# Optimization experiments

Measured on AMD Instinct MI355X. Metric: run time of the kernel, lower is better.

The kernel has to match this reference:

```python
import jax, jax.numpy as jnp
import numpy as np

N_OBJ, N_EVT, N_EDGE, N_MAIN = 50000, 100000, 500000, 25000
OBJ_DIM, EVT_DIM = 256, 256


def setup_inputs() -> dict:
    key = jax.random.key(0)
    ks = jax.random.split(key, 12)
    s = 1.0 / np.sqrt(OBJ_DIM)
    return {
        "object_X": jax.random.normal(ks[0], (N_OBJ, OBJ_DIM), jnp.float32),
        "event_X": jax.random.normal(ks[1], (N_EVT, EVT_DIM), jnp.float32),
        "lc_obj_idx": jax.random.randint(ks[2], (N_EDGE,), 0, N_OBJ),
        "lc_evt_idx": jax.random.randint(ks[3], (N_EDGE,), 0, N_EVT),
        "main_idx": jax.random.randint(ks[4], (N_MAIN,), 0, N_OBJ),
        # lifecycle_proj: Linear(event_dim, obj_dim)
        "W_proj": jax.random.uniform(ks[5], (OBJ_DIM, EVT_DIM), jnp.float32, -s, s),
        "b_proj": jax.random.uniform(ks[6], (OBJ_DIM,), jnp.float32, -s, s),
        # GRUCell(obj_dim, obj_dim): weight_ih/hh are [3*H, H]
        "W_ih": jax.random.uniform(ks[7], (3 * OBJ_DIM, OBJ_DIM), jnp.float32, -s, s),
        "b_ih": jax.random.uniform(ks[8], (3 * OBJ_DIM,), jnp.float32, -s, s),
        "W_hh": jax.random.uniform(ks[9], (3 * OBJ_DIM, OBJ_DIM), jnp.float32, -s, s),
        "b_hh": jax.random.uniform(ks[10], (3 * OBJ_DIM,), jnp.float32, -s, s),
    }


def reference(object_X, event_X, lc_obj_idx, lc_evt_idx, main_idx,
              W_proj, b_proj, W_ih, b_ih, W_hh, b_hh):
    n_obj = object_X.shape[0]
    # gather event feats, linear + ReLU  -> [E, obj_dim]
    proj = jax.nn.relu(event_X[lc_evt_idx] @ W_proj.T + b_proj)
    # scatter_mean over target objects (empty slots -> 0, like torch_scatter)
    sums = jax.ops.segment_sum(proj, lc_obj_idx, num_segments=n_obj)
    cnt = jax.ops.segment_sum(jnp.ones((lc_obj_idx.shape[0],), proj.dtype),
                              lc_obj_idx, num_segments=n_obj)
    profile = sums / jnp.maximum(cnt, 1.0)[:, None]  # [N_obj, obj_dim]
    # GRUCell(profile, object_X)
    gi = profile @ W_ih.T + b_ih   # [N_obj, 3H]
    gh = object_X @ W_hh.T + b_hh  # [N_obj, 3H]
    i_r, i_z, i_n = jnp.split(gi, 3, axis=-1)
    h_r, h_z, h_n = jnp.split(gh, 3, axis=-1)
    r = jax.nn.sigmoid(i_r + h_r)
    z = jax.nn.sigmoid(i_z + h_z)
    n = jnp.tanh(i_n + r * h_n)
    updated = (1.0 - z) * n + z * object_X
    # masked blend: only main objects take updated values
    mask = jnp.zeros((n_obj, 1), object_X.dtype).at[main_idx].set(1.0)
    return mask * updated + (1.0 - mask) * object_X
```

## Files before the change

kernel.cpp:

```cpp
#include <hip/hip_runtime.h>

typedef unsigned short u16;
typedef __attribute__((ext_vector_type(8))) short bf16x8;
typedef __attribute__((ext_vector_type(4))) float f32x4;

struct __align__(8) u16x4_t { u16 x, y, z, w; };

__device__ __forceinline__ float b2f(u16 b) {
  union { unsigned u; float f; } v; v.u = ((unsigned)b) << 16; return v.f;
}
__device__ __forceinline__ u16 f2b(float f) {
  union { float f; unsigned u; } v; v.f = f;
  unsigned r = v.u + 0x7fffu + ((v.u >> 16) & 1u);
  return (u16)(r >> 16);
}

__global__ void prep(const float* __restrict__ evtX, u16* __restrict__ evtb, int nEvtF4,
                     const float* __restrict__ Wp, const float* __restrict__ Wi,
                     const float* __restrict__ Wh, u16* __restrict__ wb,
                     const int* __restrict__ main_idx, int* __restrict__ mask,
                     int* __restrict__ mlist, int* __restrict__ cpos,
                     int* __restrict__ mcount, int nMain) {
  const int cvtBlocks = nEvtF4 / 256;
  int b = blockIdx.x;
  if (b < cvtBlocks) {
    int t = b * 256 + threadIdx.x;
    float4 v = ((const float4*)evtX)[t];
    u16x4_t o;
    o.x = f2b(v.x); o.y = f2b(v.y); o.z = f2b(v.z); o.w = f2b(v.w);
    ((u16x4_t*)evtb)[t] = o;
  } else if (b < cvtBlocks + 448) {
    int t = (b - cvtBlocks) * 256 + threadIdx.x;
    const float* src; int o;
    if (t < 16384)      { src = Wp; o = t; }
    else if (t < 65536) { src = Wi; o = t - 16384; }
    else                { src = Wh; o = t - 65536; }
    float4 v = ((const float4*)src)[o];
    u16x4_t q;
    q.x = f2b(v.x); q.y = f2b(v.y); q.z = f2b(v.z); q.w = f2b(v.w);
    ((u16x4_t*)wb)[t] = q;
  } else {
    int t = (b - cvtBlocks - 448) * 256 + threadIdx.x;
    if (t < nMain) {
      int o = main_idx[t];
      if (atomicCAS(&mask[o], 0, 1) == 0) {
        int i = atomicAdd(mcount, 1);
        mlist[i] = o;
        cpos[o] = i;
      }
    }
  }
}

__global__ void count_edges(const int* __restrict__ obj_idx, const int* __restrict__ mask,
                            int* __restrict__ deg, int n) {
  int e = blockIdx.x * 256 + threadIdx.x;
  if (e >= n) return;
  int o = obj_idx[e];
  if (mask[o]) atomicAdd(&deg[o], 1);
}

__global__ __launch_bounds__(256)
void alloc_offs(const int* __restrict__ mlist, const int* __restrict__ mcount,
                const int* __restrict__ deg, int* __restrict__ offs,
                int* __restrict__ tcur, int* __restrict__ rrows, int Mpad) {
  int i = blockIdx.x * 256 + threadIdx.x;
  int lane = threadIdx.x & 63;
  int mc = *mcount;
  if (i < Mpad) rrows[i] = (i < mc) ? mlist[i] : 0;
  int o = (i < mc) ? mlist[i] : 0;
  int d = (i < mc) ? deg[o] : 0;
  int x = d;
#pragma unroll
  for (int s = 1; s < 64; s <<= 1) {
    int y = __shfl_up(x, s, 64);
    if (lane >= s) x += y;
  }
  int wt = __shfl(x, 63, 64);
  int base = 0;
  if (lane == 63 && wt > 0) base = atomicAdd(tcur, wt);
  base = __shfl(base, 63, 64);
  if (i < mc) offs[o] = base + (x - d);
}

__global__ void fill_edges(const int* __restrict__ obj_idx, const int* __restrict__ evt_idx,
                           const int* __restrict__ mask, const int* __restrict__ offs,
                           int* __restrict__ cursor, int* __restrict__ elist, int n) {
  int e = blockIdx.x * 256 + threadIdx.x;
  if (e >= n) return;
  int o = obj_idx[e];
  if (!mask[o]) return;
  int pos = atomicAdd(&cursor[o], 1);
  elist[offs[o] + pos] = evt_idx[e];
}

__global__ __launch_bounds__(256)
void accum_gather(const u16* __restrict__ P, const int* __restrict__ elist,
                  const int* __restrict__ offs, const int* __restrict__ deg,
                  const int* __restrict__ mlist, const int* __restrict__ mcount,
                  const float* __restrict__ objX, const int* __restrict__ rrows,
                  u16* __restrict__ prof, u16* __restrict__ objc, int Mpad) {
  const int wave = threadIdx.x >> 6;
  const int lane = threadIdx.x & 63;
  const int i = blockIdx.x * 4 + wave;
  if (i >= Mpad) return;

  int src = rrows[i];
  float4 xv = *(const float4*)(objX + (size_t)src * 256 + lane * 4);

  const int mc = *mcount;
  float a0 = 0.f, a1 = 0.f, a2 = 0.f, a3 = 0.f;
  int d = 0;
  if (i < mc) {
    const int o = mlist[i];
    const int off = offs[o];
    d = deg[o];
    int j = 0;
    for (; j + 1 < d; j += 2) {
      int e0 = elist[off + j], e1 = elist[off + j + 1];
      u16x4_t p0 = *(const u16x4_t*)(P + (size_t)e0 * 256 + lane * 4);
      u16x4_t p1 = *(const u16x4_t*)(P + (size_t)e1 * 256 + lane * 4);
      a0 += b2f(p0.x) + b2f(p1.x);
      a1 += b2f(p0.y) + b2f(p1.y);
      a2 += b2f(p0.z) + b2f(p1.z);
      a3 += b2f(p0.w) + b2f(p1.w);
    }
    if (j < d) {
      int e0 = elist[off + j];
      u16x4_t p0 = *(const u16x4_t*)(P + (size_t)e0 * 256 + lane * 4);
      a0 += b2f(p0.x); a1 += b2f(p0.y); a2 += b2f(p0.z); a3 += b2f(p0.w);
    }
  }
  float s = 1.f / fmaxf((float)d, 1.f);
  u16x4_t pv;
  pv.x = f2b(a0 * s); pv.y = f2b(a1 * s); pv.z = f2b(a2 * s); pv.w = f2b(a3 * s);
  *(u16x4_t*)(prof + (size_t)i * 256 + lane * 4) = pv;

  u16x4_t ov;
  ov.x = f2b(xv.x); ov.y = f2b(xv.y); ov.z = f2b(xv.z); ov.w = f2b(xv.w);
  *(u16x4_t*)(objc + (size_t)i * 256 + lane * 4) = ov;
}

template<int RELU>
__device__ __forceinline__
void gemm_core(const u16* __restrict__ A, const u16* __restrict__ B,
               const float* __restrict__ bias, u16* __restrict__ C,
               int M, int N, int n0, int m0, u16* lA, u16* lB) {
  const int tid  = threadIdx.x;
  const int lane = tid & 63;
  const int wave = tid >> 6;
  const int mR = (wave & 1) * 64;
  const int nC = (wave >> 1) * 64;

  int srow[4], skq[4];
#pragma unroll
  for (int s = 0; s < 4; ++s) {
    int g = s * 256 + tid;
    srow[s] = g >> 3;
    skq[s]  = ((g & 7) ^ ((g >> 3) & 7)) << 3;
  }

  f32x4 acc[4][4] = {};

  auto STAGE = [&](int buf, int kt) {
#pragma unroll
    for (int s = 0; s < 4; ++s) {
      int row = srow[s];
      int ar = m0 + row; ar = (ar < M) ? ar : (M - 1);
      const u16* gA = A + (size_t)ar * 256 + kt + skq[s];
      __builtin_amdgcn_global_load_lds(
          (const __attribute__((address_space(1))) void*)gA,
          (__attribute__((address_space(3))) void*)(lA + buf * 8192 + s * 2048 + wave * 512),
          16, 0, 0);
      const u16* gB = B + (size_t)(n0 + row) * 256 + kt + skq[s];
      __builtin_amdgcn_global_load_lds(
          (const __attribute__((address_space(1))) void*)gB,
          (__attribute__((address_space(3))) void*)(lB + buf * 8192 + s * 2048 + wave * 512),
          16, 0, 0);
    }
  };

  STAGE(0, 0);
  __syncthreads();

  for (int t = 0; t < 4; ++t) {
    const int cur = t & 1;
    if (t < 3) STAGE(cur ^ 1, (t + 1) * 64);
    const u16* bA = lA + cur * 8192;
    const u16* bB = lB + cur * 8192;
#pragma unroll
    for (int ks = 0; ks < 2; ++ks) {
      const int kbq = ks * 4 + (lane >> 4);
      bf16x8 af[4], bf[4];
#pragma unroll
      for (int i = 0; i < 4; ++i) {
        int ra = mR + i * 16 + (lane & 15);
        af[i] = *(const bf16x8*)(bA + ra * 64 + ((kbq ^ (ra & 7)) << 3));
        int rb = nC + i * 16 + (lane & 15);
        bf[i] = *(const bf16x8*)(bB + rb * 64 + ((kbq ^ (rb & 7)) << 3));
      }
#pragma unroll
      for (int i = 0; i < 4; ++i)
#pragma unroll
        for (int j = 0; j < 4; ++j)
          acc[i][j] = __builtin_amdgcn_mfma_f32_16x16x32_bf16(af[i], bf[j], acc[i][j], 0, 0, 0);
    }
    __syncthreads();
  }

  const int crow = (lane >> 4) * 4;
  const int ccol = lane & 15;
#pragma unroll
  for (int i = 0; i < 4; ++i) {
#pragma unroll
    for (int j = 0; j < 4; ++j) {
      int col = n0 + nC + j * 16 + ccol;
      float bv = bias[col];
#pragma unroll
      for (int q = 0; q < 4; ++q) {
        int row = m0 + mR + i * 16 + crow + q;
        if (row < M) {
          float v = acc[i][j][q] + bv;
          if (RELU) v = fmaxf(v, 0.f);
          C[(size_t)row * N + col] = f2b(v);
        }
      }
    }
  }
}

__device__ __forceinline__ int xcd_swz(int bid, int nwg) {
  int q = nwg >> 3, r = nwg & 7;
  int xcd = bid & 7, loc = bid >> 3;
  return (xcd < r ? xcd * (q + 1) : r * (q + 1) + (xcd - r) * q) + loc;
}

__global__ __launch_bounds__(256, 2)
void gemm_p(const u16* __restrict__ A, const u16* __restrict__ B,
            const float* __restrict__ bias, u16* __restrict__ C, int M, int nwg) {
  __shared__ u16 lA[2 * 8192];
  __shared__ u16 lB[2 * 8192];
  int wg = xcd_swz(blockIdx.x, nwg);
  gemm_core<1>(A, B, bias, C, M, 256, (wg & 1) * 128, (wg >> 1) * 128, lA, lB);
}

__global__ __launch_bounds__(256, 2)
void gemm2_dual(const u16* __restrict__ prof, const u16* __restrict__ objc,
                const u16* __restrict__ wib, const u16* __restrict__ whb,
                const float* __restrict__ bi, const float* __restrict__ bh,
                u16* __restrict__ gi, u16* __restrict__ gh, int Mpad, int nwg) {
  __shared__ u16 lA[2 * 8192];
  __shared__ u16 lB[2 * 8192];
  int wg = xcd_swz(blockIdx.x, nwg);
  int m0 = (wg / 12) * 128;
  int y = wg % 12;
  if (y < 6) gemm_core<0>(prof, wib, bi, gi, Mpad, 768, y * 128, m0, lA, lB);
  else       gemm_core<0>(objc, whb, bh, gh, Mpad, 768, (y - 6) * 128, m0, lA, lB);
}

__global__ __launch_bounds__(256)
void gate_out(const u16* __restrict__ gi, const u16* __restrict__ gh,
              const float* __restrict__ objX, const int* __restrict__ mask,
              const int* __restrict__ cpos, float* __restrict__ out, int nObj) {
  const int wave = threadIdx.x >> 6;
  const int lane = threadIdx.x & 63;
  const int row = blockIdx.x * 4 + wave;
  if (row >= nObj) return;
  float4 x4 = *(const float4*)(objX + (size_t)row * 256 + lane * 4);
  float4 r4 = x4;
  if (mask[row]) {
    size_t b = (size_t)cpos[row] * 768 + lane * 4;
    u16x4_t ir = *(const u16x4_t*)(gi + b);
    u16x4_t iz = *(const u16x4_t*)(gi + b + 256);
    u16x4_t in_ = *(const u16x4_t*)(gi + b + 512);
    u16x4_t hr = *(const u16x4_t*)(gh + b);
    u16x4_t hz = *(const u16x4_t*)(gh + b + 256);
    u16x4_t hn = *(const u16x4_t*)(gh + b + 512);
    float xs[4] = {x4.x, x4.y, x4.z, x4.w};
    u16 irs[4] = {ir.x, ir.y, ir.z, ir.w};
    u16 izs[4] = {iz.x, iz.y, iz.z, iz.w};
    u16 ins[4] = {in_.x, in_.y, in_.z, in_.w};
    u16 hrs[4] = {hr.x, hr.y, hr.z, hr.w};
    u16 hzs[4] = {hz.x, hz.y, hz.z, hz.w};
    u16 hns[4] = {hn.x, hn.y, hn.z, hn.w};
    float rs[4];
#pragma unroll
    for (int q = 0; q < 4; ++q) {
      float r = 1.f / (1.f + __expf(-(b2f(irs[q]) + b2f(hrs[q]))));
      float z = 1.f / (1.f + __expf(-(b2f(izs[q]) + b2f(hzs[q]))));
      float a = b2f(ins[q]) + r * b2f(hns[q]);
      float n = 1.f - 2.f / (__expf(2.f * a) + 1.f);
      rs[q] = (1.f - z) * n + z * xs[q];
    }
    r4.x = rs[0]; r4.y = rs[1]; r4.z = rs[2]; r4.w = rs[3];
  }
  *(float4*)(out + (size_t)row * 256 + lane * 4) = r4;
}


extern "C" void kernel_launch(void* const* d_in, const int* in_sizes, int n_in,
                              void* d_out, int out_size, void* d_ws, size_t ws_size,
                              hipStream_t stream) {
  const float* objX   = (const float*)d_in[0];
  const float* evtX   = (const float*)d_in[1];
  const int* obj_idx  = (const int*)d_in[2];
  const int* evt_idx  = (const int*)d_in[3];
  const int* main_idx = (const int*)d_in[4];
  const float* Wp = (const float*)d_in[5];
  const float* bp = (const float*)d_in[6];
  const float* Wi = (const float*)d_in[7];
  const float* bi = (const float*)d_in[8];
  const float* Wh = (const float*)d_in[9];
  const float* bh = (const float*)d_in[10];

  const int nObj  = in_sizes[0] / 256;
  const int nEvt  = in_sizes[1] / 256;
  const int nEdge = in_sizes[2];
  const int nMain = in_sizes[4];
  const int Mpad  = ((nMain + 127) / 128) * 128;

  char* ws = (char*)d_ws;
  u16*   P     = (u16*)(ws + 0);
  u16*   gi    = (u16*)(ws + 0);
  u16*   gh    = (u16*)(ws + 51200000);
  u16*   prof  = (u16*)(ws + 89735168);
  u16*   objc  = (u16*)(ws + 102580224);
  u16*   evtb  = (u16*)(ws + 115425280);
  u16*   wb    = (u16*)(ws + 166625280);
  u16*   wpb   = wb;
  u16*   wib   = wb + 65536;
  u16*   whb   = wb + 262144;
  int*   deg   = (int*)(ws + 167542784);
  int*   cursor= (int*)(ws + 167742784);
  int*   mask  = (int*)(ws + 167942784);
  int*   mcount= (int*)(ws + 168142784);
  int*   tcur  = (int*)(ws + 168142848);
  int*   cpos  = (int*)(ws + 168142912);
  int*   offs  = (int*)(ws + 168342912);
  int*   mlist = (int*)(ws + 168542912);
  int*   rrows = (int*)(ws + 168643264);
  int*   elist = (int*)(ws + 168743616);
  float* out   = (float*)d_out;

  hipMemsetAsync(ws + 167542784, 0, 600128, stream);

  const int nEvtF4 = in_sizes[1] / 4;
  const int prepGrid = nEvtF4 / 256 + 448 + (nMain + 255) / 256;
  prep<<<prepGrid, 256, 0, stream>>>(evtX, evtb, nEvtF4, Wp, Wi, Wh, wb,
                                     main_idx, mask, mlist, cpos, mcount, nMain);

  const int nwgP = ((nEvt + 127) / 128) * 2;
  gemm_p<<<nwgP, 256, 0, stream>>>(evtb, wpb, bp, P, nEvt, nwgP);

  count_edges<<<(nEdge + 255) / 256, 256, 0, stream>>>(obj_idx, mask, deg, nEdge);
  alloc_offs<<<Mpad / 256, 256, 0, stream>>>(mlist, mcount, deg, offs, tcur, rrows, Mpad);
  fill_edges<<<(nEdge + 255) / 256, 256, 0, stream>>>(obj_idx, evt_idx, mask, offs, cursor, elist, nEdge);

  accum_gather<<<(Mpad + 3) / 4, 256, 0, stream>>>(P, elist, offs, deg, mlist, mcount,
                                                   objX, rrows, prof, objc, Mpad);

  const int nwg = (Mpad / 128) * 12;
  gemm2_dual<<<nwg, 256, 0, stream>>>(prof, objc, wib, whb, bi, bh, gi, gh, Mpad, nwg);

  gate_out<<<(nObj + 3) / 4, 256, 0, stream>>>(gi, gh, objX, mask, cpos, out, nObj);
}
```

Measured before the change: 389.8 us.

## Fuse fp32-to-bf16 event conversion into the projection GEMM A-load

Measured after the change: 379.7 us. 2.6% less time.

```diff
diff --git a/kernel.cpp b/kernel.cpp
--- a/kernel.cpp
+++ b/kernel.cpp
@@ -14,23 +14,20 @@
   unsigned r = v.u + 0x7fffu + ((v.u >> 16) & 1u);
   return (u16)(r >> 16);
 }
-
-__global__ void prep(const float* __restrict__ evtX, u16* __restrict__ evtb, int nEvtF4,
-                     const float* __restrict__ Wp, const float* __restrict__ Wi,
+__device__ __forceinline__ unsigned pk2(float lo, float hi) {
+  unsigned r;
+  asm("v_cvt_pk_bf16_f32 %0, %1, %2" : "=v"(r) : "v"(lo), "v"(hi));
+  return r;
+}
+
+__global__ void prep(const float* __restrict__ Wp, const float* __restrict__ Wi,
                      const float* __restrict__ Wh, u16* __restrict__ wb,
                      const int* __restrict__ main_idx, int* __restrict__ mask,
                      int* __restrict__ mlist, int* __restrict__ cpos,
                      int* __restrict__ mcount, int nMain) {
-  const int cvtBlocks = nEvtF4 / 256;
   int b = blockIdx.x;
-  if (b < cvtBlocks) {
+  if (b < 448) {
     int t = b * 256 + threadIdx.x;
-    float4 v = ((const float4*)evtX)[t];
-    u16x4_t o;
-    o.x = f2b(v.x); o.y = f2b(v.y); o.z = f2b(v.z); o.w = f2b(v.w);
-    ((u16x4_t*)evtb)[t] = o;
-  } else if (b < cvtBlocks + 448) {
-    int t = (b - cvtBlocks) * 256 + threadIdx.x;
     const float* src; int o;
     if (t < 16384)      { src = Wp; o = t; }
     else if (t < 65536) { src = Wi; o = t - 16384; }
@@ -40,7 +37,7 @@
     q.x = f2b(v.x); q.y = f2b(v.y); q.z = f2b(v.z); q.w = f2b(v.w);
     ((u16x4_t*)wb)[t] = q;
   } else {
-    int t = (b - cvtBlocks - 448) * 256 + threadIdx.x;
+    int t = (b - 448) * 256 + threadIdx.x;
     if (t < nMain) {
       int o = main_idx[t];
       if (atomicCAS(&mask[o], 0, 1) == 0) {
@@ -236,12 +233,113 @@
 }
 
 __global__ __launch_bounds__(256, 2)
-void gemm_p(const u16* __restrict__ A, const u16* __restrict__ B,
-            const float* __restrict__ bias, u16* __restrict__ C, int M, int nwg) {
+void gemm_pf(const float* __restrict__ A, const u16* __restrict__ B,
+             const float* __restrict__ bias, u16* __restrict__ C, int M, int nwg) {
   __shared__ u16 lA[2 * 8192];
   __shared__ u16 lB[2 * 8192];
   int wg = xcd_swz(blockIdx.x, nwg);
-  gemm_core<1>(A, B, bias, C, M, 256, (wg & 1) * 128, (wg >> 1) * 128, lA, lB);
+  const int n0 = (wg & 1) * 128;
+  const int m0 = (wg >> 1) * 128;
+
+  const int tid  = threadIdx.x;
+  const int lane = tid & 63;
+  const int wave = tid >> 6;
+  const int mR = (wave & 1) * 64;
+  const int nC = (wave >> 1) * 64;
+
+  const float* aptr[4];
+  int sdst[4], skq[4], srow[4];
+#pragma unroll
+  for (int s = 0; s < 4; ++s) {
+    int g = s * 256 + tid;
+    int row = g >> 3, q = g & 7;
+    srow[s] = row;
+    sdst[s] = row * 64 + ((q ^ (row & 7)) << 3);
+    skq[s]  = (q ^ (row & 7)) << 3;
+    int ar = m0 + row; ar = (ar < M) ? ar : (M - 1);
+    aptr[s] = A + (size_t)ar * 256 + q * 8;
+  }
+
+  f32x4 acc[4][4] = {};
+  float4 fa[4][2];
+
+  auto LOAD_A = [&](int kt) {
+#pragma unroll
+    for (int s = 0; s < 4; ++s) {
+      fa[s][0] = *(const float4*)(aptr[s] + kt);
+      fa[s][1] = *(const float4*)(aptr[s] + kt + 4);
+    }
+  };
+  auto WRITE_A = [&](int buf) {
+#pragma unroll
+    for (int s = 0; s < 4; ++s) {
+      uint4 w;
+      w.x = pk2(fa[s][0].x, fa[s][0].y);
+      w.y = pk2(fa[s][0].z, fa[s][0].w);
+      w.z = pk2(fa[s][1].x, fa[s][1].y);
+      w.w = pk2(fa[s][1].z, fa[s][1].w);
+      *(uint4*)(lA + buf * 8192 + sdst[s]) = w;
+    }
+  };
+  auto STAGE_B = [&](int buf, int kt) {
+#pragma unroll
+    for (int s = 0; s < 4; ++s) {
+      const u16* gB = B + (size_t)(n0 + srow[s]) * 256 + kt + skq[s];
+      __builtin_amdgcn_global_load_lds(
+          (const __attribute__((address_space(1))) void*)gB,
+          (__attribute__((address_space(3))) void*)(lB + buf * 8192 + s * 2048 + wave * 512),
+          16, 0, 0);
+    }
+  };
+
+  LOAD_A(0); STAGE_B(0, 0);
+  WRITE_A(0);
+  __syncthreads();
+
+  for (int t = 0; t < 4; ++t) {
+    const int cur = t & 1;
+    if (t < 3) { LOAD_A((t + 1) * 64); STAGE_B(cur ^ 1, (t + 1) * 64); }
+    const u16* bA = lA + cur * 8192;
+    const u16* bB = lB + cur * 8192;
+#pragma unroll
+    for (int ks = 0; ks < 2; ++ks) {
+      const int kbq = ks * 4 + (lane >> 4);
+      bf16x8 af[4], bf[4];
+#pragma unroll
+      for (int i = 0; i < 4; ++i) {
+        int ra = mR + i * 16 + (lane & 15);
+        af[i] = *(const bf16x8*)(bA + ra * 64 + ((kbq ^ (ra & 7)) << 3));
+        int rb = nC + i * 16 + (lane & 15);
+        bf[i] = *(const bf16x8*)(bB + rb * 64 + ((kbq ^ (rb & 7)) << 3));
+      }
+#pragma unroll
+      for (int i = 0; i < 4; ++i)
+#pragma unroll
+        for (int j = 0; j < 4; ++j)
+          acc[i][j] = __builtin_amdgcn_mfma_f32_16x16x32_bf16(af[i], bf[j], acc[i][j], 0, 0, 0);
+    }
+    if (t < 3) WRITE_A(cur ^ 1);
+    __syncthreads();
+  }
+
+  const int crow = (lane >> 4) * 4;
+  const int ccol = lane & 15;
+#pragma unroll
+  for (int i = 0; i < 4; ++i) {
+#pragma unroll
+    for (int j = 0; j < 4; ++j) {
+      int col = n0 + nC + j * 16 + ccol;
+      float bv = bias[col];
+#pragma unroll
+      for (int q = 0; q < 4; ++q) {
+        int row = m0 + mR + i * 16 + crow + q;
+        if (row < M) {
+          float v = acc[i][j][q] + bv;
+          C[(size_t)row * 256 + col] = f2b(fmaxf(v, 0.f));
+        }
+      }
+    }
+  }
 }
 
 __global__ __launch_bounds__(256, 2)
@@ -325,7 +423,6 @@
   u16*   gh    = (u16*)(ws + 51200000);
   u16*   prof  = (u16*)(ws + 89735168);
   u16*   objc  = (u16*)(ws + 102580224);
-  u16*   evtb  = (u16*)(ws + 115425280);
   u16*   wb    = (u16*)(ws + 166625280);
   u16*   wpb   = wb;
   u16*   wib   = wb + 65536;
@@ -344,13 +441,12 @@
 
   hipMemsetAsync(ws + 167542784, 0, 600128, stream);
 
-  const int nEvtF4 = in_sizes[1] / 4;
-  const int prepGrid = nEvtF4 / 256 + 448 + (nMain + 255) / 256;
-  prep<<<prepGrid, 256, 0, stream>>>(evtX, evtb, nEvtF4, Wp, Wi, Wh, wb,
+  const int prepGrid = 448 + (nMain + 255) / 256;
+  prep<<<prepGrid, 256, 0, stream>>>(Wp, Wi, Wh, wb,
                                      main_idx, mask, mlist, cpos, mcount, nMain);
 
   const int nwgP = ((nEvt + 127) / 128) * 2;
-  gemm_p<<<nwgP, 256, 0, stream>>>(evtb, wpb, bp, P, nEvt, nwgP);
+  gemm_pf<<<nwgP, 256, 0, stream>>>(evtX, wpb, bp, P, nEvt, nwgP);
 
   count_edges<<<(nEdge + 255) / 256, 256, 0, stream>>>(obj_idx, mask, deg, nEdge);
   alloc_offs<<<Mpad / 256, 256, 0, stream>>>(mlist, mcount, deg, offs, tcur, rrows, Mpad);
```
